# Kernel optimization log

Hardware: AMD Instinct MI355X
Metric: run time of the kernel (lower is better)

The kernel has to match this reference:

```python
import jax, jax.numpy as jnp
import numpy as np

SEG_LENS = (2048, 4096, 8192)
DIL_RATES = (1, 2, 4)
NUM_HEADS = 12
HEAD_DIM = 64
LN_EPS = 1e-5


def _dilated_attention(q, k, v):
    # q,k,v: [b, n, h, d]; heads partitioned across (segment, dilation) groups
    b, n, h, d = q.shape
    G = len(SEG_LENS)
    hg = h // G
    scale = d ** -0.5
    out = jnp.zeros_like(q)
    for i, (s, r) in enumerate(zip(SEG_LENS, DIL_RATES)):
        hmin = i * hg
        m = n // s                      # number of segments
        idx = jnp.arange(i % r, s, r)   # dilated positions within a segment, len = s // r
        def seg(t):
            # [b, n, hg, d] -> [b, m, s//r, hg, d]
            return t[:, :, hmin:hmin + hg, :].reshape(b, m, s, hg, d)[:, :, idx]
        qs, ks, vs = seg(q), seg(k), seg(v)
        scores = jnp.einsum('bmshd,bmthd->bmhst', qs, ks) * scale  # [b,m,hg,s/r,s/r]
        attn = jax.nn.softmax(scores, axis=-1)
        o = jnp.einsum('bmhst,bmthd->bmshd', attn, vs)              # [b,m,s/r,hg,d]
        pos = (jnp.arange(m)[:, None] * s + idx[None, :]).reshape(-1)
        out = out.at[:, pos, hmin:hmin + hg, :].set(o.reshape(b, -1, hg, d))
    return out


def setup_inputs() -> dict:
    key = jax.random.key(0)
    ks = jax.random.split(key, 4)
    E = NUM_HEADS * HEAD_DIM
    b, n = 1, 8192
    x = jax.random.normal(ks[0], (b, n, E), dtype=jnp.float32)
    w_qkv = jax.random.normal(ks[1], (3 * E, E), dtype=jnp.float32) * (E ** -0.5)
    b_qkv = jnp.zeros((3 * E,), dtype=jnp.float32)
    w_out = jax.random.normal(ks[2], (E, E), dtype=jnp.float32) * (E ** -0.5)
    b_out = jnp.zeros((E,), dtype=jnp.float32)
    ln_gamma = jnp.ones((E,), dtype=jnp.float32)
    ln_beta = jnp.zeros((E,), dtype=jnp.float32)
    return {'x': x, 'w_qkv': w_qkv, 'b_qkv': b_qkv, 'w_out': w_out,
            'b_out': b_out, 'ln_gamma': ln_gamma, 'ln_beta': ln_beta}


def reference(x, w_qkv, b_qkv, w_out, b_out, ln_gamma, ln_beta):
    b, n, E = x.shape
    qkv = x @ w_qkv.T + b_qkv
    q, k, v = jnp.split(qkv, 3, axis=-1)
    shp = (b, n, NUM_HEADS, HEAD_DIM)
    o = _dilated_attention(q.reshape(shp), k.reshape(shp), v.reshape(shp)).reshape(b, n, E)
    # MAGNETO: LayerNorm on attention output before out projection
    mu = jnp.mean(o, axis=-1, keepdims=True)
    var = jnp.mean(jnp.square(o - mu), axis=-1, keepdims=True)
    on = (o - mu) / jnp.sqrt(var + LN_EPS) * ln_gamma + ln_beta
    return on @ w_out.T + b_out
```

## Files before the change

### kernel.cpp

```cpp
#include <hip/hip_runtime.h>
#include <hip/hip_bf16.h>
#include <cstdint>
#include <cstddef>


typedef __attribute__((ext_vector_type(8))) short short8;
typedef __attribute__((ext_vector_type(4))) short short4_;
typedef __attribute__((ext_vector_type(4))) float float4_;
typedef __attribute__((ext_vector_type(16))) float floatx16;
typedef __attribute__((ext_vector_type(4))) int int4_;

#if __has_builtin(__builtin_amdgcn_exp2f)
#define EXP2(x) __builtin_amdgcn_exp2f(x)
#else
#define EXP2(x) exp2f(x)
#endif

#define QK_SCALE 0.1803368801111244f

__device__ __forceinline__ float bf2f(short s) {
    unsigned int u = ((unsigned int)(unsigned short)s) << 16;
    float f;
    __builtin_memcpy(&f, &u, 4);
    return f;
}
__device__ __forceinline__ short f2bf(float f) {
    unsigned int u;
    __builtin_memcpy(&u, &f, 4);
    u += 0x7fffu + ((u >> 16) & 1u);
    return (short)(u >> 16);
}
__device__ __forceinline__ short8 f8_to_bf8_s(const float* __restrict__ p, float s) {
    float4_ a = *(const float4_*)(p);
    float4_ b = *(const float4_*)(p + 4);
    short8 r;
    r[0] = f2bf(a[0] * s); r[1] = f2bf(a[1] * s);
    r[2] = f2bf(a[2] * s); r[3] = f2bf(a[3] * s);
    r[4] = f2bf(b[0] * s); r[5] = f2bf(b[1] * s);
    r[6] = f2bf(b[2] * s); r[7] = f2bf(b[3] * s);
    return r;
}
__device__ __forceinline__ void gll16(const short* g, short* l) {
    __builtin_amdgcn_global_load_lds(
        (const __attribute__((address_space(1))) unsigned int*)g,
        (__attribute__((address_space(3))) unsigned int*)l, 16, 0, 0);
}
__device__ __forceinline__ int cvtpk(float lo, float hi) {
    int r;
    asm("v_cvt_pk_bf16_f32 %0, %1, %2" : "=v"(r) : "v"(lo), "v"(hi));
    return r;
}

#define LDT 72

__global__ __launch_bounds__(256) void cvt3(
    const float* __restrict__ a, int na, const float* __restrict__ b, int nb,
    const float* __restrict__ c, int nc,
    short* __restrict__ oa, short* __restrict__ ob, short* __restrict__ oc)
{
    int i = (blockIdx.x * 256 + threadIdx.x) * 8;
    if (i < na) {
        *(short8*)&oa[i] = f8_to_bf8_s(a + i, 1.0f);
    } else if (i < na + nb) {
        int j = i - na;
        float s = (j >= 768 * 768 && j < 1536 * 768) ? QK_SCALE : 1.0f;
        *(short8*)&ob[j] = f8_to_bf8_s(b + j, s);
    } else {
        int j = i - na - nb;
        if (j < nc) *(short8*)&oc[j] = f8_to_bf8_s(c + j, 1.0f);
    }
}

__global__ __launch_bounds__(256) void gemm_qkv(
    const short* __restrict__ A,
    const short* __restrict__ B,
    const float* __restrict__ bias,
    short* __restrict__ C)
{
    __shared__ short As[128 * 64];
    __shared__ short Bs[64 * 64];

    const int bx = blockIdx.x;
    const int L  = (bx & 7) * 168 + (bx >> 3);
    int g, t, rate, off0;
    if (L < 768)       { g = 0; t = L;        rate = 1; off0 = 0; }
    else if (L < 1152) { g = 1; t = L - 768;  rate = 2; off0 = 1; }
    else               { g = 2; t = L - 1152; rate = 4; off0 = 2; }
    const int nx = t % 12, my = t / 12;
    const int ncol0 = (nx >> 2) * 768 + g * 256 + (nx & 3) * 64;
    const int m0 = my * 128;
    const float bscale = ((nx >> 2) == 1) ? QK_SCALE : 1.0f;

    const int tid  = threadIdx.x;
    const int wave = tid >> 6, lane = tid & 63;
    const int quad = lane >> 4, l16 = lane & 15;
    const int lrow   = lane >> 3;
    const int lchunk = (lane & 7) ^ lrow;

    const short* Abase = A + (size_t)(off0 + (m0 + wave * 32 + lrow) * rate) * 768
                           + lchunk * 8;
    const short* Bbase = B + (size_t)(ncol0 + wave * 16 + lrow) * 768 + lchunk * 8;
    short* AsW = &As[(wave * 32) * 64];
    short* BsW = &Bs[(wave * 16) * 64];
    const size_t arowstep = (size_t)8 * rate * 768;

    float4_ acc[2][4] = {};

    for (int k0 = 0; k0 < 768; k0 += 64) {
        __syncthreads();
        #pragma unroll
        for (int i = 0; i < 4; i++)
            gll16(Abase + (size_t)i * arowstep + k0, AsW + (i * 8) * 64);
        #pragma unroll
        for (int i = 0; i < 2; i++)
            gll16(Bbase + (size_t)(i * 8) * 768 + k0, BsW + (i * 8) * 64);
        __syncthreads();
        #pragma unroll
        for (int ks = 0; ks < 2; ks++) {
            const int ca = ((ks * 4 + quad) ^ (l16 & 7)) * 8;
            short8 af[2], bf[4];
            #pragma unroll
            for (int mt = 0; mt < 2; mt++)
                af[mt] = *(const short8*)&As[(wave * 32 + mt * 16 + l16) * 64 + ca];
            #pragma unroll
            for (int nt = 0; nt < 4; nt++)
                bf[nt] = *(const short8*)&Bs[(nt * 16 + l16) * 64 + ca];
            #pragma unroll
            for (int mt = 0; mt < 2; mt++)
                #pragma unroll
                for (int nt = 0; nt < 4; nt++)
                    acc[mt][nt] = __builtin_amdgcn_mfma_f32_16x16x32_bf16(
                        af[mt], bf[nt], acc[mt][nt], 0, 0, 0);
        }
    }

    #pragma unroll
    for (int nt = 0; nt < 4; nt++) {
        const int gcol = ncol0 + nt * 16 + l16;
        const float bv = bias[gcol] * bscale;
        #pragma unroll
        for (int mt = 0; mt < 2; mt++) {
            #pragma unroll
            for (int r = 0; r < 4; r++) {
                const int rl = m0 + wave * 32 + mt * 16 + quad * 4 + r;
                const size_t grow = (size_t)off0 + (size_t)rl * rate;
                C[grow * 2304 + gcol] = f2bf(acc[mt][nt][r] + bv);
            }
        }
    }
}

__global__ __launch_bounds__(256) void gemm_out(
    const short* __restrict__ A,
    const short* __restrict__ B,
    const float* __restrict__ bias,
    float* __restrict__ C)
{
    __shared__ short As[128 * 64];
    __shared__ short Bs[64 * 64];

    const int bx = blockIdx.x;
    const int L  = (bx & 7) * 96 + (bx >> 3);
    const int nx = L % 12, my = L / 12;
    const int n0 = nx * 64, m0 = my * 128;

    const int tid  = threadIdx.x;
    const int wave = tid >> 6, lane = tid & 63;
    const int quad = lane >> 4, l16 = lane & 15;
    const int lrow   = lane >> 3;
    const int lchunk = (lane & 7) ^ lrow;

    const short* Abase = A + (size_t)(m0 + wave * 32 + lrow) * 2304 + lchunk * 8;
    const short* Bbase = B + (size_t)(n0 + wave * 16 + lrow) * 768 + lchunk * 8;
    short* AsW = &As[(wave * 32) * 64];
    short* BsW = &Bs[(wave * 16) * 64];

    float4_ acc[2][4] = {};

    for (int k0 = 0; k0 < 768; k0 += 64) {
        __syncthreads();
        #pragma unroll
        for (int i = 0; i < 4; i++)
            gll16(Abase + (size_t)(i * 8) * 2304 + k0, AsW + (i * 8) * 64);
        #pragma unroll
        for (int i = 0; i < 2; i++)
            gll16(Bbase + (size_t)(i * 8) * 768 + k0, BsW + (i * 8) * 64);
        __syncthreads();
        #pragma unroll
        for (int ks = 0; ks < 2; ks++) {
            const int ca = ((ks * 4 + quad) ^ (l16 & 7)) * 8;
            short8 af[2], bf[4];
            #pragma unroll
            for (int mt = 0; mt < 2; mt++)
                af[mt] = *(const short8*)&As[(wave * 32 + mt * 16 + l16) * 64 + ca];
            #pragma unroll
            for (int nt = 0; nt < 4; nt++)
                bf[nt] = *(const short8*)&Bs[(nt * 16 + l16) * 64 + ca];
            #pragma unroll
            for (int mt = 0; mt < 2; mt++)
                #pragma unroll
                for (int nt = 0; nt < 4; nt++)
                    acc[mt][nt] = __builtin_amdgcn_mfma_f32_16x16x32_bf16(
                        af[mt], bf[nt], acc[mt][nt], 0, 0, 0);
        }
    }

    #pragma unroll
    for (int nt = 0; nt < 4; nt++) {
        const int col = n0 + nt * 16 + l16;
        const float bv = bias[col];
        #pragma unroll
        for (int mt = 0; mt < 2; mt++) {
            #pragma unroll
            for (int r = 0; r < 4; r++) {
                const int row = m0 + wave * 32 + mt * 16 + quad * 4 + r;
                C[(size_t)row * 768 + col] = acc[mt][nt][r] + bv;
            }
        }
    }
}

__global__ __launch_bounds__(256, 4) void dilated_attn(
    const short* __restrict__ qkv, short* __restrict__ obuf1,
    short* __restrict__ obuf2, float* __restrict__ lbuf)
{
    __shared__ short Ks[2 * 64 * 64];
    __shared__ short Vt[2 * 64 * LDT];

    const int bx = blockIdx.x;
    const int L  = (bx & 7) * 112 + (bx >> 3);
    const int qt   = L & 15;
    const int half = (L >> 4) & 1;
    const int sh   = L >> 5;

    int g, seg, s, rate, off0;
    if (sh < 16)      { g = 0; seg = sh >> 2;        s = 2048; rate = 1; off0 = 0; }
    else if (sh < 24) { g = 1; seg = (sh - 16) >> 2; s = 4096; rate = 2; off0 = 1; }
    else              { g = 2; seg = 0;              s = 8192; rate = 4; off0 = 2; }
    const int head = g * 4 + (sh & 3);

    const int tid  = threadIdx.x;
    const int wave = tid >> 6, lane = tid & 63;
    const int h = lane >> 5, l32 = lane & 31;
    const int srow = tid >> 2, scol = (tid & 3) * 16;

    const size_t bpos = (size_t)seg * s + off0
                      + (size_t)(qt * 128 + wave * 32) * rate;
    short8 aq[4];
    {
        const short* qsrc = qkv + (bpos + (size_t)l32 * rate) * 2304
                                + head * 64 + h * 8;
        #pragma unroll
        for (int kt = 0; kt < 4; kt++)
            aq[kt] = *(const short8*)(qsrc + kt * 16);
    }

    const int krow0  = wave * 8 + (lane >> 3);
    const int kchunk = (lane & 7) ^ (lane >> 3);
    const size_t kstep = (size_t)64 * rate * 2304;
    const size_t kq0 = (size_t)seg * s + off0 + (size_t)(half * 1024) * rate;
    const short* kg0 = qkv + (kq0 + (size_t)krow0 * rate) * 2304
                           + 768 + head * 64 + kchunk * 8;
    const short* kg1 = kg0 + (size_t)32 * rate * 2304;
    const short* vgp = qkv + (kq0 + (size_t)srow * rate) * 2304
                           + 1536 + head * 64 + scol;
    const int kofsA = (wave * 8) * 64;
    const int kofsB = kofsA + 32 * 64;
    const int vswz  = scol;

    gll16(kg0, &Ks[kofsA]);
    gll16(kg1, &Ks[kofsB]);
    kg0 += kstep; kg1 += kstep;
    short8 va0 = *(const short8*)(vgp);
    short8 va1 = *(const short8*)(vgp + 8);
    vgp += kstep;
    #pragma unroll
    for (int e = 0; e < 8; e++) Vt[(scol + e) * LDT + (srow ^ vswz)] = va0[e];
    #pragma unroll
    for (int e = 0; e < 8; e++) Vt[(scol + 8 + e) * LDT + (srow ^ vswz)] = va1[e];
    va0 = *(const short8*)(vgp);
    va1 = *(const short8*)(vgp + 8);
    vgp += kstep;

    float lsum = 0.f;
    floatx16 oacc[2] = {};

    auto compute = [&](const short* kb, const short* vb) {
        floatx16 sacc[2] = {};
        __builtin_amdgcn_s_setprio(1);
        #pragma unroll
        for (int kt = 0; kt < 4; kt++) {
            #pragma unroll
            for (int t = 0; t < 2; t++) {
                short8 ak = *(const short8*)&kb[(t * 32 + l32) * 64
                                                + (((kt * 2 + h) ^ (l32 & 7)) * 8)];
                sacc[t] = __builtin_amdgcn_mfma_f32_32x32x16_bf16(
                    ak, aq[kt], sacc[t], 0, 0, 0);
            }
        }
        __builtin_amdgcn_s_setprio(0);

        #pragma unroll
        for (int e = 0; e < 16; e++) {
            float pa_ = EXP2(sacc[0][e]);
            float pb_ = EXP2(sacc[1][e]);
            sacc[0][e] = pa_; sacc[1][e] = pb_;
            lsum += pa_ + pb_;
        }

        short8 pa[4];
        #pragma unroll
        for (int kt = 0; kt < 4; kt++) {
            const int t = kt >> 1, b = (kt & 1) * 8;
            int A1 = cvtpk(sacc[t][b + 0], sacc[t][b + 1]);
            int A2 = cvtpk(sacc[t][b + 2], sacc[t][b + 3]);
            int B1 = cvtpk(sacc[t][b + 4], sacc[t][b + 5]);
            int B2 = cvtpk(sacc[t][b + 6], sacc[t][b + 7]);
            asm volatile("v_permlane32_swap_b32 %0, %1" : "+v"(A1), "+v"(B1));
            asm volatile("v_permlane32_swap_b32 %0, %1" : "+v"(A2), "+v"(B2));
            int4_ w; w[0] = A1; w[1] = A2; w[2] = B1; w[3] = B2;
            __builtin_memcpy(&pa[kt], &w, 16);
        }

        __builtin_amdgcn_s_setprio(1);
        #pragma unroll
        for (int kt = 0; kt < 4; kt++) {
            #pragma unroll
            for (int dt = 0; dt < 2; dt++) {
                const int d = dt * 32 + l32;
                short8 bv = *(const short8*)&vb[d * LDT
                                                + ((kt ^ ((d >> 4) & 3)) * 16 + h * 8)];
                oacc[dt] = __builtin_amdgcn_mfma_f32_32x32x16_bf16(
                    pa[kt], bv, oacc[dt], 0, 0, 0);
            }
        }
        __builtin_amdgcn_s_setprio(0);
    };

    for (int j = 0; j < 15; j++) {
        asm volatile("s_waitcnt vmcnt(2)" ::: "memory");
        asm volatile("s_waitcnt lgkmcnt(0)" ::: "memory");
        __builtin_amdgcn_s_barrier();

        const int nb = (j + 1) & 1;
        gll16(kg0, &Ks[nb * 4096 + kofsA]);
        gll16(kg1, &Ks[nb * 4096 + kofsB]);
        kg0 += kstep; kg1 += kstep;
        asm volatile("s_waitcnt vmcnt(2)" ::: "memory");
        short* vt = &Vt[nb * 64 * LDT];
        #pragma unroll
        for (int e = 0; e < 8; e++) vt[(scol + e) * LDT + (srow ^ vswz)] = va0[e];
        #pragma unroll
        for (int e = 0; e < 8; e++) vt[(scol + 8 + e) * LDT + (srow ^ vswz)] = va1[e];
        if (j < 14) {
            va0 = *(const short8*)(vgp);
            va1 = *(const short8*)(vgp + 8);
            vgp += kstep;
        }
        compute(&Ks[(j & 1) * 4096], &Vt[(j & 1) * 64 * LDT]);
    }
    asm volatile("s_waitcnt vmcnt(0)" ::: "memory");
    asm volatile("s_waitcnt lgkmcnt(0)" ::: "memory");
    __builtin_amdgcn_s_barrier();
    compute(&Ks[4096], &Vt[64 * LDT]);

    {
        short* obase = half ? obuf2 : obuf1;
        float* lb = lbuf + (size_t)half * 8192 * 12;
        float lt = lsum + __shfl_xor(lsum, 32, 64);
        #pragma unroll
        for (int m = 0; m < 4; m++) {
            #pragma unroll
            for (int r = 0; r < 4; r++) {
                const int ql = 4 * h + r + 8 * m;
                short* od = obase + (bpos + (size_t)ql * rate) * 768 + head * 64;
                od[l32]      = f2bf(oacc[0][m * 4 + r]);
                od[32 + l32] = f2bf(oacc[1][m * 4 + r]);
            }
        }
        if (lane < 32)
            lb[(bpos + (size_t)l32 * rate) * 12 + head] = lt;
    }
}

__global__ __launch_bounds__(256) void ln_inplace(
    short* __restrict__ qkv, const short* __restrict__ obuf1,
    const short* __restrict__ obuf2, const float* __restrict__ lbuf,
    const float* __restrict__ gamma, const float* __restrict__ beta)
{
    const int row  = blockIdx.x * 4 + (threadIdx.x >> 6);
    const int lane = threadIdx.x & 63;
    const short* s1 = obuf1 + (size_t)row * 768;
    const short* s2 = obuf2 + (size_t)row * 768;
    short* dst = qkv + (size_t)row * 2304;

    const int h1 = lane >> 3;
    const int h2 = 8 + (lane >> 4);
    const bool cov1 = (h1 < 4) || ((row & 1) == 1);
    const bool cov2 = ((row & 3) == 2);
    const float li1 = cov1
        ? 1.0f / (lbuf[row * 12 + h1] + lbuf[8192 * 12 + row * 12 + h1]) : 0.0f;
    const float li2 = cov2
        ? 1.0f / (lbuf[row * 12 + h2] + lbuf[8192 * 12 + row * 12 + h2]) : 0.0f;

    short8  a  = *(const short8*)&s1[lane * 8];
    short4_ b  = *(const short4_*)&s1[512 + lane * 4];
    short8  a2 = *(const short8*)&s2[lane * 8];
    short4_ b2 = *(const short4_*)&s2[512 + lane * 4];
    float v[12];
    #pragma unroll
    for (int e = 0; e < 8; e++)
        v[e] = cov1 ? (bf2f(a[e]) + bf2f(a2[e])) * li1 : 0.0f;
    #pragma unroll
    for (int e = 0; e < 4; e++)
        v[8 + e] = cov2 ? (bf2f(b[e]) + bf2f(b2[e])) * li2 : 0.0f;

    float sum = 0.f, sq = 0.f;
    #pragma unroll
    for (int e = 0; e < 12; e++) { sum += v[e]; sq += v[e] * v[e]; }
    #pragma unroll
    for (int off = 1; off < 64; off <<= 1) {
        sum += __shfl_xor(sum, off, 64);
        sq  += __shfl_xor(sq,  off, 64);
    }
    float mean = sum * (1.0f / 768.0f);
    float var  = sq * (1.0f / 768.0f) - mean * mean;
    float rstd = rsqrtf(var + 1e-5f);

    short8 o8; short4_ o4;
    #pragma unroll
    for (int e = 0; e < 8; e++)
        o8[e] = f2bf((v[e] - mean) * rstd * gamma[lane * 8 + e] + beta[lane * 8 + e]);
    #pragma unroll
    for (int e = 0; e < 4; e++)
        o4[e] = f2bf((v[8 + e] - mean) * rstd * gamma[512 + lane * 4 + e] + beta[512 + lane * 4 + e]);

    *(short8*)&dst[lane * 8] = o8;
    *(short4_*)&dst[512 + lane * 4] = o4;
}

extern "C" void kernel_launch(void* const* d_in, const int* in_sizes, int n_in,
                              void* d_out, int out_size, void* d_ws, size_t ws_size,
                              hipStream_t stream) {
    const float* x     = (const float*)d_in[0];
    const float* w_qkv = (const float*)d_in[1];
    const float* b_qkv = (const float*)d_in[2];
    const float* w_out = (const float*)d_in[3];
    const float* b_out = (const float*)d_in[4];
    const float* gamma = (const float*)d_in[5];
    const float* beta  = (const float*)d_in[6];
    float* out = (float*)d_out;

    const int NX = 8192 * 768, NW1 = 2304 * 768, NW2 = 768 * 768;
    char* ws = (char*)d_ws;
    short* qkv   = (short*)(ws);
    short* xb    = (short*)(ws + (size_t)8192 * 2304 * 2);
    short* wqkvb = xb + NX;
    short* woutb = wqkvb + NW1;
    float* lbuf  = (float*)(woutb + NW2);
    short* obuf2 = (short*)(lbuf + 2 * 8192 * 12);
    short* obuf1 = xb;

    cvt3<<<dim3((NX + NW1 + NW2) / (256 * 8)), 256, 0, stream>>>(
        x, NX, w_qkv, NW1, w_out, NW2, xb, wqkvb, woutb);

    gemm_qkv<<<dim3(1344), 256, 0, stream>>>(xb, wqkvb, b_qkv, qkv);

    dilated_attn<<<dim3(28 * 2 * 16), 256, 0, stream>>>(qkv, obuf1, obuf2, lbuf);

    ln_inplace<<<dim3(8192 / 4), 256, 0, stream>>>(
        qkv, obuf1, obuf2, lbuf, gamma, beta);

    gemm_out<<<dim3(768), 256, 0, stream>>>(qkv, woutb, b_out, out);
}
```

Baseline: 182.6 us.

## Load K fragments directly from global memory into registers, dropping K LDS staging

The K tile is no longer staged through shared memory with async global-to-LDS loads. Each wave now reads its K MFMA operand fragments straight from global memory into registers every iteration, and the QK MFMA loop is reordered to accumulate per tile. This removes LDS traffic and the LDS footprint for K, which may raise occupancy. In exchange K loads are issued at the start of each iteration with no prefetch depth, so global latency may be exposed, and each of the four waves now fetches K separately.

After: 203.4 us. 1.11x slower.

```diff
diff --git a/kernel.cpp b/kernel.cpp
--- a/kernel.cpp
+++ b/kernel.cpp
@@ -224,7 +224,6 @@
     const short* __restrict__ qkv, short* __restrict__ obuf1,
     short* __restrict__ obuf2, float* __restrict__ lbuf)
 {
-    __shared__ short Ks[2 * 64 * 64];
     __shared__ short Vt[2 * 64 * LDT];
 
     const int bx = blockIdx.x;
@@ -255,22 +254,15 @@
             aq[kt] = *(const short8*)(qsrc + kt * 16);
     }
 
-    const int krow0  = wave * 8 + (lane >> 3);
-    const int kchunk = (lane & 7) ^ (lane >> 3);
     const size_t kstep = (size_t)64 * rate * 2304;
+    const size_t krow32 = (size_t)32 * rate * 2304;
     const size_t kq0 = (size_t)seg * s + off0 + (size_t)(half * 1024) * rate;
-    const short* kg0 = qkv + (kq0 + (size_t)krow0 * rate) * 2304
-                           + 768 + head * 64 + kchunk * 8;
-    const short* kg1 = kg0 + (size_t)32 * rate * 2304;
+    const short* kb = qkv + (kq0 + (size_t)l32 * rate) * 2304
+                          + 768 + head * 64 + h * 8;
     const short* vgp = qkv + (kq0 + (size_t)srow * rate) * 2304
                            + 1536 + head * 64 + scol;
-    const int kofsA = (wave * 8) * 64;
-    const int kofsB = kofsA + 32 * 64;
-    const int vswz  = scol;
-
-    gll16(kg0, &Ks[kofsA]);
-    gll16(kg1, &Ks[kofsB]);
-    kg0 += kstep; kg1 += kstep;
+    const int vswz = scol;
+
     short8 va0 = *(const short8*)(vgp);
     short8 va1 = *(const short8*)(vgp + 8);
     vgp += kstep;
@@ -285,18 +277,17 @@
     float lsum = 0.f;
     floatx16 oacc[2] = {};
 
-    auto compute = [&](const short* kb, const short* vb) {
-        floatx16 sacc[2] = {};
+    auto compute = [&](const short* vb, const short8* kf) {
+        floatx16 sacc[2];
         __builtin_amdgcn_s_setprio(1);
         #pragma unroll
-        for (int kt = 0; kt < 4; kt++) {
-            #pragma unroll
-            for (int t = 0; t < 2; t++) {
-                short8 ak = *(const short8*)&kb[(t * 32 + l32) * 64
-                                                + (((kt * 2 + h) ^ (l32 & 7)) * 8)];
-                sacc[t] = __builtin_amdgcn_mfma_f32_32x32x16_bf16(
-                    ak, aq[kt], sacc[t], 0, 0, 0);
-            }
+        for (int t = 0; t < 2; t++) {
+            floatx16 sc = {};
+            #pragma unroll
+            for (int kt = 0; kt < 4; kt++)
+                sc = __builtin_amdgcn_mfma_f32_32x32x16_bf16(
+                    kf[t * 4 + kt], aq[kt], sc, 0, 0, 0);
+            sacc[t] = sc;
         }
         __builtin_amdgcn_s_setprio(0);
 
@@ -338,31 +329,42 @@
     };
 
     for (int j = 0; j < 15; j++) {
-        asm volatile("s_waitcnt vmcnt(2)" ::: "memory");
+        short8 kf[8];
+        #pragma unroll
+        for (int t = 0; t < 2; t++)
+            #pragma unroll
+            for (int kt = 0; kt < 4; kt++)
+                kf[t * 4 + kt] = *(const short8*)(kb + (size_t)t * krow32 + kt * 16);
+        kb += kstep;
+
         asm volatile("s_waitcnt lgkmcnt(0)" ::: "memory");
         __builtin_amdgcn_s_barrier();
+        asm volatile("" ::: "memory");
 
         const int nb = (j + 1) & 1;
-        gll16(kg0, &Ks[nb * 4096 + kofsA]);
-        gll16(kg1, &Ks[nb * 4096 + kofsB]);
-        kg0 += kstep; kg1 += kstep;
-        asm volatile("s_waitcnt vmcnt(2)" ::: "memory");
         short* vt = &Vt[nb * 64 * LDT];
         #pragma unroll
         for (int e = 0; e < 8; e++) vt[(scol + e) * LDT + (srow ^ vswz)] = va0[e];
         #pragma unroll
         for (int e = 0; e < 8; e++) vt[(scol + 8 + e) * LDT + (srow ^ vswz)] = va1[e];
-        if (j < 14) {
-            va0 = *(const short8*)(vgp);
-            va1 = *(const short8*)(vgp + 8);
-            vgp += kstep;
-        }
-        compute(&Ks[(j & 1) * 4096], &Vt[(j & 1) * 64 * LDT]);
-    }
-    asm volatile("s_waitcnt vmcnt(0)" ::: "memory");
-    asm volatile("s_waitcnt lgkmcnt(0)" ::: "memory");
-    __builtin_amdgcn_s_barrier();
-    compute(&Ks[4096], &Vt[64 * LDT]);
+        va0 = *(const short8*)(vgp);
+        va1 = *(const short8*)(vgp + 8);
+        if (j < 14) vgp += kstep;
+
+        compute(&Vt[(j & 1) * 64 * LDT], kf);
+    }
+    {
+        short8 kf[8];
+        #pragma unroll
+        for (int t = 0; t < 2; t++)
+            #pragma unroll
+            for (int kt = 0; kt < 4; kt++)
+                kf[t * 4 + kt] = *(const short8*)(kb + (size_t)t * krow32 + kt * 16);
+        asm volatile("s_waitcnt lgkmcnt(0)" ::: "memory");
+        __builtin_amdgcn_s_barrier();
+        asm volatile("" ::: "memory");
+        compute(&Vt[64 * LDT], kf);
+    }
 
     {
         short* obase = half ? obuf2 : obuf1;
```
